# Optimization experiments

Hardware: AMD Instinct MI355X
Metric: run time of the kernel (lower is better)

Reference implementation:

```python
import jax, jax.numpy as jnp
import numpy as np

N = 65536          # number of input vectors
D = 128            # embedding_dim
K = 2048           # num_embeddings (codebook size)
DH = D // 2        # linear_proj output dim


def setup_inputs() -> dict:
    key = jax.random.key(0)
    k1, k2, k3, k4 = jax.random.split(key, 4)
    z = jax.random.normal(k1, (N, D), dtype=jnp.float32)
    # linear_proj params (nn.Linear(D, D//2)): weight [DH, D], bias [DH]
    W = jax.random.normal(k2, (DH, D), dtype=jnp.float32) * (1.0 / np.sqrt(D))
    b = jax.random.normal(k3, (DH,), dtype=jnp.float32) * 0.01
    # codebook buffer, initialized ~ N(0,1) as in the torch module
    embeddings = jax.random.normal(k4, (K, D), dtype=jnp.float32)
    return {"z": z, "W": W, "b": b, "embeddings": embeddings}


def reference(z, W, b, embeddings):
    # project inputs and codebook into half-dim space
    z_ = z @ W.T + b                       # [N, DH]
    emb_ = embeddings @ W.T + b            # [K, DH]
    # squared euclidean distances via ||a||^2 + ||b||^2 - 2 a.b
    distances = ((z_ ** 2).sum(-1, keepdims=True)
                 + (emb_ ** 2).sum(-1)
                 - 2.0 * (z_ @ emb_.T))    # [N, K]
    closest = jnp.argmin(distances, axis=-1)               # [N]
    one_hot_encoding = jax.nn.one_hot(closest, K, dtype=jnp.float32)  # [N, K]
    quantized = one_hot_encoding @ embeddings               # [N, D] (gather)
    return (quantized, one_hot_encoding)
```

## Files before the change

kernel.cpp:

```cpp
#include <hip/hip_runtime.h>
#include <float.h>

#define N_ROWS 65536
#define D_IN   128
#define DH     64
#define K_CB   2048

typedef const __attribute__((address_space(1))) void* gas_p;
typedef __attribute__((address_space(3))) void* las_p;
typedef _Float16 f16x8 __attribute__((ext_vector_type(8)));
typedef float    f32x4 __attribute__((ext_vector_type(4)));

__global__ __launch_bounds__(256) void k_project(
    const float* __restrict__ Z, const float* __restrict__ emb,
    const float* __restrict__ W, const float* __restrict__ b,
    _Float16* __restrict__ zpl,
    _Float16* __restrict__ epl,
    float* __restrict__ e2,
    float* __restrict__ outOH) {
  __shared__ __align__(16) float Wl[64 * 140];
  __shared__ __align__(16) float Zl[16 * 128];
  int tid = threadIdx.x;
  const float* src; _Float16* dst; int n0; bool do_e2; size_t plane;
  if ((int)blockIdx.x < 4096) {
    src = Z;   dst = zpl; n0 = blockIdx.x * 16;          do_e2 = false; plane = (size_t)N_ROWS * 64;
  } else {
    src = emb; dst = epl; n0 = (blockIdx.x - 4096) * 16; do_e2 = true;  plane = (size_t)K_CB * 64;
  }

#pragma unroll
  for (int i = 0; i < 8; ++i) {
    int idx4 = tid + 256 * i;
    int j = idx4 >> 5;
    int d4 = (idx4 & 31) * 4;
    *(float4*)&Wl[j * 140 + d4] = *(const float4*)(W + j * 128 + d4);
  }
#pragma unroll
  for (int i = 0; i < 2; ++i) {
    int idx4 = tid + 256 * i;
    int r = idx4 >> 5;
    int d4 = (idx4 & 31) * 4;
    *(float4*)&Zl[r * 128 + d4] = *(const float4*)(src + (size_t)(n0 + r) * 128 + d4);
  }
  int j = tid & 63, g = tid >> 6;
  float bj = b[j];
  __syncthreads();

  if (outOH && (int)blockIdx.x < 4096) {
    f32x4 zz4 = (f32x4){0.f, 0.f, 0.f, 0.f};
    f32x4* dz = (f32x4*)(outOH + (size_t)n0 * K_CB);
#pragma unroll
    for (int i = 0; i < 32; ++i)
      __builtin_nontemporal_store(zz4, dz + tid + 256 * i);
  }

  float acc[4] = {0.f, 0.f, 0.f, 0.f};
  for (int d4 = 0; d4 < 128; d4 += 4) {
    float4 w4 = *(float4*)&Wl[j * 140 + d4];
#pragma unroll
    for (int i = 0; i < 4; ++i) {
      float4 z4 = *(float4*)&Zl[(g * 4 + i) * 128 + d4];
      acc[i] = fmaf(z4.x, w4.x, fmaf(z4.y, w4.y, fmaf(z4.z, w4.z, fmaf(z4.w, w4.w, acc[i]))));
    }
  }
#pragma unroll
  for (int i = 0; i < 4; ++i) {
    int n = n0 + g * 4 + i;
    float v = acc[i] + bj;
    _Float16 h = (_Float16)v;  float rm = v - (float)h;
    _Float16 m = (_Float16)rm;
    int pos = (((j >> 3) ^ (n & 7)) << 3) | (j & 7);
    size_t base = (size_t)n * 64 + pos;
    dst[base]         = h;
    dst[plane + base] = m;
    if (do_e2) {
      float s = v * v;
#pragma unroll
      for (int off = 32; off > 0; off >>= 1) s += __shfl_xor(s, off, 64);
      if (j == 0) e2[n] = s;
    }
  }
}

__global__ __launch_bounds__(256, 2) void k_score(
    const _Float16* __restrict__ zpl,
    const _Float16* __restrict__ epl,
    const float* __restrict__ e2,
    const float* __restrict__ emb,
    float* __restrict__ outQ,
    float* __restrict__ outOH,
    int* __restrict__ cidx_g) {
  __shared__ __align__(16) char U[65536];
  _Float16* Zs  = (_Float16*)U;
  char*     es0 = U + 32768;
  char*     es1 = U + 49152;
  __shared__ int cidxs[128];

  int tid = threadIdx.x, lane = tid & 63, wid = tid >> 6;
  int quad = lane >> 4, l16 = lane & 15;
  int row0 = blockIdx.x * 128;

  for (int q = wid; q < 32; q += 4) {
    int p = q >> 4, within = (q & 15) * 1024;
    const char* g = (const char*)zpl + (size_t)p * ((size_t)N_ROWS * 128)
                  + (size_t)row0 * 128 + within + lane * 16;
    __builtin_amdgcn_global_load_lds((gas_p)g, (las_p)((char*)Zs + p * 16384 + within), 16, 0, 0);
  }
  for (int q = wid; q < 16; q += 4) {
    int p = q >> 3, within = (q & 7) * 1024;
    const char* g = (const char*)epl + (size_t)p * (K_CB * 128) + within + lane * 16;
    __builtin_amdgcn_global_load_lds((gas_p)g, (las_p)(es0 + p * 8192 + within), 16, 0, 0);
  }

  __syncthreads();

  f16x8 A[2][4][2];
#pragma unroll
  for (int step = 0; step < 2; ++step)
#pragma unroll
    for (int mt = 0; mt < 4; ++mt) {
      int tr = mt * 16 + l16;
      int cph = (step * 4 + quad) ^ (tr & 7);
      const _Float16* pa = Zs + tr * 64 + cph * 8;
      A[step][mt][0] = *(const f16x8*)pa;
      A[step][mt][1] = *(const f16x8*)(pa + 8192);
    }

  float best[32]; int bidx[32];
#pragma unroll
  for (int s = 0; s < 32; ++s) { best[s] = FLT_MAX; bidx[s] = 0; }

  for (int t = 0; t < 32; ++t) {
    const _Float16* esc = (const _Float16*)((t & 1) ? es1 : es0);
    if (t < 31) {
      char* esn = (t & 1) ? es0 : es1;
      for (int q = wid; q < 16; q += 4) {
        int p = q >> 3, within = (q & 7) * 1024;
        const char* g = (const char*)epl + (size_t)p * (K_CB * 128)
                      + (size_t)(t + 1) * 8192 + within + lane * 16;
        __builtin_amdgcn_global_load_lds((gas_p)g, (las_p)(esn + p * 8192 + within), 16, 0, 0);
      }
    }
    int col = t * 64 + wid * 16 + l16;
    float ev = e2[col];

    f32x4 acc0[4], acc1[4];
#pragma unroll
    for (int mt = 0; mt < 4; ++mt) {
      acc0[mt] = (f32x4){0.f, 0.f, 0.f, 0.f};
      acc1[mt] = (f32x4){0.f, 0.f, 0.f, 0.f};
    }

#pragma unroll
    for (int step = 0; step < 2; ++step) {
      int tc = wid * 16 + l16;
      int cph = (step * 4 + quad) ^ (l16 & 7);
      const _Float16* pb = esc + tc * 64 + cph * 8;
      f16x8 Bh = *(const f16x8*)pb;
      f16x8 Bm = *(const f16x8*)(pb + 4096);
#pragma unroll
      for (int mt = 0; mt < 4; ++mt) {
        f32x4 c = acc0[mt];
        c = __builtin_amdgcn_mfma_f32_16x16x32_f16(A[step][mt][1], Bm, c, 0, 0, 0);
        c = __builtin_amdgcn_mfma_f32_16x16x32_f16(A[step][mt][1], Bh, c, 0, 0, 0);
        c = __builtin_amdgcn_mfma_f32_16x16x32_f16(A[step][mt][0], Bm, c, 0, 0, 0);
        c = __builtin_amdgcn_mfma_f32_16x16x32_f16(A[step][mt][0], Bh, c, 0, 0, 0);
        acc0[mt] = c;
      }
#pragma unroll
      for (int mt = 0; mt < 4; ++mt) {
        int tr = 64 + mt * 16 + l16;
        int cph1 = (step * 4 + quad) ^ (tr & 7);
        const _Float16* pa = Zs + tr * 64 + cph1 * 8;
        f16x8 Ah = *(const f16x8*)pa;
        f16x8 Am = *(const f16x8*)(pa + 8192);
        f32x4 c = acc1[mt];
        c = __builtin_amdgcn_mfma_f32_16x16x32_f16(Am, Bm, c, 0, 0, 0);
        c = __builtin_amdgcn_mfma_f32_16x16x32_f16(Am, Bh, c, 0, 0, 0);
        c = __builtin_amdgcn_mfma_f32_16x16x32_f16(Ah, Bm, c, 0, 0, 0);
        c = __builtin_amdgcn_mfma_f32_16x16x32_f16(Ah, Bh, c, 0, 0, 0);
        acc1[mt] = c;
      }
    }

#pragma unroll
    for (int mt = 0; mt < 4; ++mt)
#pragma unroll
      for (int r = 0; r < 4; ++r) {
        float s0 = fmaf(-2.0f, acc0[mt][r], ev);
        int slot = mt * 4 + r;
        if (s0 < best[slot]) { best[slot] = s0; bidx[slot] = col; }
        float s1 = fmaf(-2.0f, acc1[mt][r], ev);
        if (s1 < best[16 + slot]) { best[16 + slot] = s1; bidx[16 + slot] = col; }
      }

    __syncthreads();
  }

  float* redm = (float*)U;
  int*   redi = (int*)(U + 32768);
#pragma unroll
  for (int grp = 0; grp < 2; ++grp)
#pragma unroll
    for (int mt = 0; mt < 4; ++mt)
#pragma unroll
      for (int r = 0; r < 4; ++r) {
        int row = grp * 64 + mt * 16 + quad * 4 + r;
        redm[row * 64 + wid * 16 + l16] = best[grp * 16 + mt * 4 + r];
        redi[row * 64 + wid * 16 + l16] = bidx[grp * 16 + mt * 4 + r];
      }
  __syncthreads();
  if (tid < 128) {
    float m = redm[tid * 64]; int mi = redi[tid * 64];
    for (int s = 1; s < 64; ++s) {
      float v = redm[tid * 64 + s]; int vi = redi[tid * 64 + s];
      if (v < m || (v == m && vi < mi)) { m = v; mi = vi; }
    }
    cidxs[tid] = mi;
  }
  __syncthreads();

  if (outOH) {
    if (tid < 128) outOH[(size_t)(row0 + tid) * K_CB + cidxs[tid]] = 1.0f;
  } else {
    if (tid < 128) cidx_g[row0 + tid] = cidxs[tid];
  }

#pragma unroll
  for (int i = 0; i < 16; ++i) {
    int idx = tid + 256 * i;
    int r = idx >> 5, c = (idx & 31) * 4;
    f32x4 v = *(const f32x4*)(emb + (size_t)cidxs[r] * D_IN + c);
    __builtin_nontemporal_store(v, (f32x4*)(outQ + (size_t)(row0 + r) * D_IN + c));
  }
}

__global__ void k_epilogue(const int* __restrict__ cidx_g, float* __restrict__ outOH) {
  int tid  = threadIdx.x;
  int row0 = blockIdx.x * 64;
  float4 zz4 = make_float4(0.f, 0.f, 0.f, 0.f);
  for (int r = 0; r < 64; ++r) {
    float4* dst = (float4*)(outOH + (size_t)(row0 + r) * K_CB);
    dst[tid]       = zz4;
    dst[tid + 256] = zz4;
  }
  __syncthreads();
  if (tid < 64) {
    int r = row0 + tid;
    outOH[(size_t)r * K_CB + cidx_g[r]] = 1.0f;
  }
}

extern "C" void kernel_launch(void* const* d_in, const int* in_sizes, int n_in,
                              void* d_out, int out_size, void* d_ws, size_t ws_size,
                              hipStream_t stream) {
  (void)in_sizes; (void)n_in; (void)out_size;
  const float* Z   = (const float*)d_in[0];
  const float* W   = (const float*)d_in[1];
  const float* b   = (const float*)d_in[2];
  const float* emb = (const float*)d_in[3];
  float* outQ  = (float*)d_out;
  float* outOH = (float*)d_out + (size_t)N_ROWS * D_IN;

  char* wsb = (char*)d_ws;
  _Float16* epl = (_Float16*)wsb;
  float*    e2  = (float*)(wsb + 524288);
  const size_t need_primary = 524288 + 8192 + (size_t)2 * N_ROWS * 64 * 2;

  if (ws_size >= need_primary) {
    _Float16* zpl = (_Float16*)(wsb + 532480);
    k_project<<<4224, 256, 0, stream>>>(Z, emb, W, b, zpl, epl, e2, outOH);
    k_score<<<512, 256, 0, stream>>>(zpl, epl, e2, emb, outQ, outOH, nullptr);
  } else {
    int*      cidx_g = (int*)(wsb + 532480);
    _Float16* zpl    = (_Float16*)outOH;
    k_project<<<4224, 256, 0, stream>>>(Z, emb, W, b, zpl, epl, e2, nullptr);
    k_score<<<512, 256, 0, stream>>>(zpl, epl, e2, emb, outQ, nullptr, cidx_g);
    k_epilogue<<<1024, 256, 0, stream>>>(cidx_g, outOH);
  }
}
```

Measured before the change: 664.6 us.

## Triple-buffer codebook tiles with single barrier per iteration and prefetch distance two

Replaces the double-buffered codebook staging in LDS with a three-slot ring, issuing loads two tiles ahead and waiting with explicit vmcnt counts instead of a trailing __syncthreads. The squared-norm values are preloaded into registers up front, and the tile loop is fully unrolled. The aim is to hide global-to-LDS latency and remove one barrier per iteration. In exchange, LDS use grows to 80KB per block and register pressure rises, which could affect occupancy or cause spills.

```diff
diff --git a/kernel.cpp b/kernel.cpp
--- a/kernel.cpp
+++ b/kernel.cpp
@@ -90,15 +90,16 @@
     float* __restrict__ outQ,
     float* __restrict__ outOH,
     int* __restrict__ cidx_g) {
-  __shared__ __align__(16) char U[65536];
-  _Float16* Zs  = (_Float16*)U;
-  char*     es0 = U + 32768;
-  char*     es1 = U + 49152;
-  __shared__ int cidxs[128];
+  __shared__ __align__(16) char U[81920];
+  _Float16* Zs = (_Float16*)U;
 
   int tid = threadIdx.x, lane = tid & 63, wid = tid >> 6;
   int quad = lane >> 4, l16 = lane & 15;
   int row0 = blockIdx.x * 128;
+
+  float e2r[32];
+#pragma unroll
+  for (int t = 0; t < 32; ++t) e2r[t] = e2[t * 64 + wid * 16 + l16];
 
   for (int q = wid; q < 32; q += 4) {
     int p = q >> 4, within = (q & 15) * 1024;
@@ -106,13 +107,20 @@
                   + (size_t)row0 * 128 + within + lane * 16;
     __builtin_amdgcn_global_load_lds((gas_p)g, (las_p)((char*)Zs + p * 16384 + within), 16, 0, 0);
   }
-  for (int q = wid; q < 16; q += 4) {
-    int p = q >> 3, within = (q & 7) * 1024;
-    const char* g = (const char*)epl + (size_t)p * (K_CB * 128) + within + lane * 16;
-    __builtin_amdgcn_global_load_lds((gas_p)g, (las_p)(es0 + p * 8192 + within), 16, 0, 0);
-  }
-
-  __syncthreads();
+#pragma unroll
+  for (int tt = 0; tt < 2; ++tt)
+    for (int q = wid; q < 16; q += 4) {
+      int p = q >> 3, within = (q & 7) * 1024;
+      const char* g = (const char*)epl + (size_t)p * (K_CB * 128)
+                    + (size_t)tt * 8192 + within + lane * 16;
+      __builtin_amdgcn_global_load_lds((gas_p)g,
+          (las_p)(U + 32768 + tt * 16384 + p * 8192 + within), 16, 0, 0);
+    }
+
+  asm volatile("s_waitcnt vmcnt(8)" ::: "memory");
+  __builtin_amdgcn_sched_barrier(0);
+  __builtin_amdgcn_s_barrier();
+  __builtin_amdgcn_sched_barrier(0);
 
   f16x8 A[2][4][2];
 #pragma unroll
@@ -130,20 +138,15 @@
 #pragma unroll
   for (int s = 0; s < 32; ++s) { best[s] = FLT_MAX; bidx[s] = 0; }
 
+#pragma unroll
   for (int t = 0; t < 32; ++t) {
-    const _Float16* esc = (const _Float16*)((t & 1) ? es1 : es0);
-    if (t < 31) {
-      char* esn = (t & 1) ? es0 : es1;
-      for (int q = wid; q < 16; q += 4) {
-        int p = q >> 3, within = (q & 7) * 1024;
-        const char* g = (const char*)epl + (size_t)p * (K_CB * 128)
-                      + (size_t)(t + 1) * 8192 + within + lane * 16;
-        __builtin_amdgcn_global_load_lds((gas_p)g, (las_p)(esn + p * 8192 + within), 16, 0, 0);
-      }
-    }
-    int col = t * 64 + wid * 16 + l16;
-    float ev = e2[col];
-
+    if (t < 31) { asm volatile("s_waitcnt vmcnt(4)" ::: "memory"); }
+    else        { asm volatile("s_waitcnt vmcnt(0)" ::: "memory"); }
+    __builtin_amdgcn_sched_barrier(0);
+    __builtin_amdgcn_s_barrier();
+    __builtin_amdgcn_sched_barrier(0);
+
+    const _Float16* esc = (const _Float16*)(U + 32768 + (t % 3) * 16384);
     f32x4 acc0[4], acc1[4];
 #pragma unroll
     for (int mt = 0; mt < 4; ++mt) {
@@ -183,22 +186,36 @@
       }
     }
 
-#pragma unroll
-    for (int mt = 0; mt < 4; ++mt)
-#pragma unroll
-      for (int r = 0; r < 4; ++r) {
-        float s0 = fmaf(-2.0f, acc0[mt][r], ev);
-        int slot = mt * 4 + r;
-        if (s0 < best[slot]) { best[slot] = s0; bidx[slot] = col; }
-        float s1 = fmaf(-2.0f, acc1[mt][r], ev);
-        if (s1 < best[16 + slot]) { best[16 + slot] = s1; bidx[16 + slot] = col; }
-      }
-
-    __syncthreads();
-  }
+    {
+      int col = t * 64 + wid * 16 + l16;
+      float ev = e2r[t];
+#pragma unroll
+      for (int mt = 0; mt < 4; ++mt)
+#pragma unroll
+        for (int r = 0; r < 4; ++r) {
+          float s0 = fmaf(-2.0f, acc0[mt][r], ev);
+          int slot = mt * 4 + r;
+          if (s0 < best[slot]) { best[slot] = s0; bidx[slot] = col; }
+          float s1 = fmaf(-2.0f, acc1[mt][r], ev);
+          if (s1 < best[16 + slot]) { best[16 + slot] = s1; bidx[16 + slot] = col; }
+        }
+    }
+
+    if (t < 30) {
+      char* esn = U + 32768 + ((t + 2) % 3) * 16384;
+      for (int q = wid; q < 16; q += 4) {
+        int p = q >> 3, within = (q & 7) * 1024;
+        const char* g = (const char*)epl + (size_t)p * (K_CB * 128)
+                      + (size_t)(t + 2) * 8192 + within + lane * 16;
+        __builtin_amdgcn_global_load_lds((gas_p)g, (las_p)(esn + p * 8192 + within), 16, 0, 0);
+      }
+    }
+  }
+  __syncthreads();
 
   float* redm = (float*)U;
   int*   redi = (int*)(U + 32768);
+  int*   cidx = (int*)(U + 65536);
 #pragma unroll
   for (int grp = 0; grp < 2; ++grp)
 #pragma unroll
@@ -216,21 +233,21 @@
       float v = redm[tid * 64 + s]; int vi = redi[tid * 64 + s];
       if (v < m || (v == m && vi < mi)) { m = v; mi = vi; }
     }
-    cidxs[tid] = mi;
+    cidx[tid] = mi;
   }
   __syncthreads();
 
   if (outOH) {
-    if (tid < 128) outOH[(size_t)(row0 + tid) * K_CB + cidxs[tid]] = 1.0f;
+    if (tid < 128) outOH[(size_t)(row0 + tid) * K_CB + cidx[tid]] = 1.0f;
   } else {
-    if (tid < 128) cidx_g[row0 + tid] = cidxs[tid];
+    if (tid < 128) cidx_g[row0 + tid] = cidx[tid];
   }
 
 #pragma unroll
   for (int i = 0; i < 16; ++i) {
     int idx = tid + 256 * i;
     int r = idx >> 5, c = (idx & 31) * 4;
-    f32x4 v = *(const f32x4*)(emb + (size_t)cidxs[r] * D_IN + c);
+    f32x4 v = *(const f32x4*)(emb + (size_t)cidx[r] * D_IN + c);
     __builtin_nontemporal_store(v, (f32x4*)(outQ + (size_t)(row0 + r) * D_IN + c));
   }
 }
```

Measured after the change: 1.248 ms. 87.8% more time.
